# Optimization experiments

Hardware: AMD Instinct MI355X
Metric: run time of the kernel (lower is better)

The kernel has to match this reference:

```python
import jax, jax.numpy as jnp
import numpy as np

N, E, H, L = 50000, 600000, 128, 4  # nodes, edges, hidden_dim, num_layers


def setup_inputs() -> dict:
    key = jax.random.key(0)
    ks = jax.random.split(key, 12)
    def w(k, shape):
        fan_in = shape[-2]
        return jax.random.normal(k, shape, jnp.float32) / np.float32(np.sqrt(fan_in))
    return {
        "loc": jax.random.normal(ks[0], (N, 3), jnp.float32),
        "vel": jax.random.normal(ks[1], (N, 3), jnp.float32),
        "edge_attr": jax.random.normal(ks[2], (E, 2), jnp.float32),
        "row": jax.random.randint(ks[3], (E,), 0, N),
        "col": jax.random.randint(ks[4], (E,), 0, N),
        # embedding: Linear(6 -> H)
        "emb_w": w(ks[5], (6, H)), "emb_b": jnp.zeros((H,), jnp.float32),
        # per-layer edge MLP: Linear(2H+2 -> H), SiLU, Linear(H -> H), SiLU
        "ew1": w(ks[6], (L, 2 * H + 2, H)), "eb1": jnp.zeros((L, H), jnp.float32),
        "ew2": w(ks[7], (L, H, H)), "eb2": jnp.zeros((L, H), jnp.float32),
        # per-layer node MLP: Linear(2H -> H), SiLU, Linear(H -> H)
        "nw1": w(ks[8], (L, 2 * H, H)), "nb1": jnp.zeros((L, H), jnp.float32),
        "nw2": w(ks[9], (L, H, H)), "nb2": jnp.zeros((L, H), jnp.float32),
        # decoder: Linear(H -> H), SiLU, Linear(H -> 3)
        "dw1": w(ks[10], (H, H)), "db1": jnp.zeros((H,), jnp.float32),
        "dw2": w(ks[11], (H, 3)), "db2": jnp.zeros((3,), jnp.float32),
    }


def reference(loc, vel, edge_attr, row, col, emb_w, emb_b, ew1, eb1, ew2, eb2,
              nw1, nb1, nw2, nb2, dw1, db1, dw2, db2):
    silu = jax.nn.silu
    # embedding of [loc, vel]
    h = jnp.concatenate([loc, vel], axis=1) @ emb_w + emb_b  # [N, H]
    for i in range(L):
        # edge model: gather endpoints, concat edge_attr, 2-layer SiLU MLP
        e_in = jnp.concatenate([h[row], h[col], edge_attr], axis=1)  # [E, 2H+2]
        m = silu(silu(e_in @ ew1[i] + eb1[i]) @ ew2[i] + eb2[i])     # [E, H]
        # node model: scatter-sum messages into source nodes (row), MLP, residual
        agg = jax.ops.segment_sum(m, row, num_segments=N)            # [N, H]
        upd = silu(jnp.concatenate([h, agg], axis=1) @ nw1[i] + nb1[i]) @ nw2[i] + nb2[i]
        h = h + upd  # recurrent=True
    return silu(h @ dw1 + db1) @ dw2 + db2  # [N, 3]
```

## Files before the change

kernel.cpp:

```cpp
#include <hip/hip_runtime.h>

#define NN 50000
#define NE 600000
#define HD 128
#define NL 4
#define NSCB 196

typedef __bf16 bf16x8 __attribute__((ext_vector_type(8)));
typedef float f32x4 __attribute__((ext_vector_type(4)));

__device__ __forceinline__ unsigned short f2bf(float x){
  union { float f; unsigned int u; } v; v.f = x;
  unsigned int r = v.u + 0x7FFFu + ((v.u >> 16) & 1u);
  return (unsigned short)(r >> 16);
}
__device__ __forceinline__ float silu_f(float x){
  float e, r;
  float t = x * -1.44269504088896340736f;
  asm("v_exp_f32 %0, %1" : "=v"(e) : "v"(t));
  float d = 1.f + e;
  asm("v_rcp_f32 %0, %1" : "=v"(r) : "v"(d));
  return x * r;
}
__device__ __forceinline__ unsigned pk_bf16(float v0, float v1){
  unsigned r;
  asm("v_cvt_pk_bf16_f32 %0, %1, %2" : "=v"(r) : "v"(v0), "v"(v1));
  return r;
}

__device__ __forceinline__ f32x4 mfma_b16(bf16x8 a, bf16x8 b, f32x4 c){
  return __builtin_amdgcn_mfma_f32_16x16x32_bf16(a, b, c, 0, 0, 0);
}

typedef __attribute__((address_space(1))) const unsigned int* gas1p;
typedef __attribute__((address_space(3))) unsigned int* las3p;
__device__ __forceinline__ void gll16(const void* g, void* l){
  __builtin_amdgcn_global_load_lds((gas1p)g, (las3p)l, 16, 0, 0);
}

__global__ __launch_bounds__(256) void pack_b(const float* __restrict__ src,
    unsigned short* __restrict__ dst, int K, int Klimit, int srcLayerStride, int perm){
  int layer = blockIdx.y;
  int tid = blockIdx.x*256 + threadIdx.x;
  int j = tid & 7, lane = (tid >> 3) & 63, nb = (tid >> 9) & 7, kk = tid >> 12;
  int krow = (kk << 5) + ((lane >> 4) << 3) + j;
  int ll = lane & 15;
  int c = perm ? (((((nb >> 1) << 4) + ll) << 1) + (nb & 1)) : ((nb << 4) + ll);
  float v = (krow < Klimit) ? src[(size_t)layer*srcLayerStride + krow*HD + c] : 0.f;
  dst[(size_t)layer*K*HD + tid] = f2bf(v);
}

__global__ __launch_bounds__(256) void emb_kernel(
    const float* __restrict__ loc, const float* __restrict__ vel,
    const float* __restrict__ ew, const float* __restrict__ eb,
    float* __restrict__ hf, unsigned short* __restrict__ hb)
{
  int gid = blockIdx.x*256 + threadIdx.x;
  int n = gid >> 7, j = gid & 127;
  float s = eb[j];
  s += loc[n*3+0]*ew[0*HD+j] + loc[n*3+1]*ew[1*HD+j] + loc[n*3+2]*ew[2*HD+j];
  s += vel[n*3+0]*ew[3*HD+j] + vel[n*3+1]*ew[4*HD+j] + vel[n*3+2]*ew[5*HD+j];
  hf[gid] = s;
  hb[gid] = f2bf(s);
}

__global__ __launch_bounds__(256) void count_kernel(const int* __restrict__ rowIdx, int* __restrict__ cnt){
  int e = blockIdx.x*256 + threadIdx.x;
  if (e < NE) atomicAdd(cnt + rowIdx[e], 1);
}

__global__ __launch_bounds__(256) void blocksum_kernel(const int* __restrict__ cnt, int* __restrict__ bsum){
  __shared__ int s[256];
  int t = threadIdx.x, i = blockIdx.x*256 + t;
  s[t] = (i < NN) ? cnt[i] : 0;
  __syncthreads();
  for (int d = 128; d > 0; d >>= 1){
    if (t < d) s[t] += s[t + d];
    __syncthreads();
  }
  if (t == 0) bsum[blockIdx.x] = s[0];
}

__global__ __launch_bounds__(256) void scanb_kernel(int* __restrict__ bsum){
  __shared__ int s[256];
  int t = threadIdx.x;
  int v = (t < NSCB) ? bsum[t] : 0;
  s[t] = v;
  __syncthreads();
  for (int d = 1; d < 256; d <<= 1){
    int u = (t >= d) ? s[t-d] : 0;
    __syncthreads();
    s[t] += u;
    __syncthreads();
  }
  if (t < NSCB) bsum[t] = s[t] - v;
}

__global__ __launch_bounds__(256) void offsets_kernel(const int* __restrict__ cnt,
    const int* __restrict__ bsum, int* __restrict__ cur){
  __shared__ int s[256];
  int t = threadIdx.x, i = blockIdx.x*256 + t;
  int v = (i < NN) ? cnt[i] : 0;
  s[t] = v;
  __syncthreads();
  for (int d = 1; d < 256; d <<= 1){
    int u = (t >= d) ? s[t-d] : 0;
    __syncthreads();
    s[t] += u;
    __syncthreads();
  }
  if (i < NN) cur[i] = bsum[blockIdx.x] + s[t] - v;
}

__global__ __launch_bounds__(256) void assign_kernel(
    const int* __restrict__ rowIdx, const int* __restrict__ colIdx,
    const float* __restrict__ ea, int* __restrict__ cur,
    int* __restrict__ row_s, int* __restrict__ col_s, float* __restrict__ ea_s){
  int e = blockIdx.x*256 + threadIdx.x;
  if (e < NE){
    int r = rowIdx[e];
    int s = atomicAdd(cur + r, 1);
    int s64 = s & 63;
    int sp = (s & ~63) | (((s64 >> 2) & 3) << 4) | (((s64 >> 4) & 3) << 2) | (s64 & 3);
    row_s[sp] = r;
    col_s[sp] = colIdx[e];
    ea_s[2*sp]   = ea[2*e];
    ea_s[2*sp+1] = ea[2*e+1];
  }
}

#define SWZ(a) ((a) ^ (((a) >> 4) & 0x30))

__global__ __launch_bounds__(256, 8) void edge_kernel(
    const unsigned short* __restrict__ hb,
    const int* __restrict__ row_s, const int* __restrict__ col_s,
    const float* __restrict__ ea_s,
    const unsigned short* __restrict__ B1p, const unsigned short* __restrict__ B2p,
    const float* __restrict__ bias1, const float* __restrict__ bias2,
    const float* __restrict__ wea,
    float* __restrict__ aggf)
{
  __shared__ alignas(128) char sA[1024*16];
  __shared__ int sRow[64];
  __shared__ float2 sEa[64];
  uint4* sA4 = reinterpret_cast<uint4*>(sA);

  const int t = threadIdx.x;
  const int w = t >> 6, l = t & 63, lw = l >> 4, ll = l & 15;
  const int e0 = blockIdx.x << 6;

  if (t < 64){
    sRow[t] = row_s[e0 + t];
    sEa[t] = reinterpret_cast<const float2*>(ea_s)[e0 + t];
  }
  const int er = e0 + (w << 4) + ll;
  const int nrow = row_s[er];
  const int ncol = col_s[er];
  const unsigned short* gr = hb + (size_t)nrow*HD + (lw << 3);
  #pragma unroll
  for (int kk = 0; kk < 4; ++kk)
    gll16(gr + (kk << 5), sA + ((size_t)(((kk << 2) + w)) << 10));
  asm volatile("s_waitcnt vmcnt(0)" ::: "memory");
  __syncthreads();

  const int q2 = ((w << 4) + ll) << 1;
  const float2 bb1 = *reinterpret_cast<const float2*>(bias1 + q2);
  const float2 wA = *reinterpret_cast<const float2*>(wea + q2);
  const float2 wB = *reinterpret_cast<const float2*>(wea + HD + q2);

  f32x4 acc[4][2] = {};
  #pragma unroll
  for (int kk = 0; kk < 4; ++kk){
    bf16x8 a[4], b[2];
    #pragma unroll
    for (int r = 0; r < 4; ++r)
      a[r] = *reinterpret_cast<const bf16x8*>(&sA4[((kk << 2) + r)*64 + l]);
    #pragma unroll
    for (int c = 0; c < 2; ++c)
      b[c] = *reinterpret_cast<const bf16x8*>(B1p + ((((kk << 3) + (w << 1) + c) << 6) + l)*8);
    #pragma unroll
    for (int r = 0; r < 4; ++r)
      #pragma unroll
      for (int c = 0; c < 2; ++c)
        acc[r][c] = mfma_b16(a[r], b[c], acc[r][c]);
  }
  __syncthreads();

  const unsigned short* gc = hb + (size_t)ncol*HD + (lw << 3);
  #pragma unroll
  for (int kk = 0; kk < 4; ++kk)
    gll16(gc + (kk << 5), sA + ((size_t)(((kk << 2) + w)) << 10));
  asm volatile("s_waitcnt vmcnt(0)" ::: "memory");
  __syncthreads();

  #pragma unroll
  for (int kk = 4; kk < 8; ++kk){
    bf16x8 a[4], b[2];
    #pragma unroll
    for (int r = 0; r < 4; ++r)
      a[r] = *reinterpret_cast<const bf16x8*>(&sA4[(((kk - 4) << 2) + r)*64 + l]);
    #pragma unroll
    for (int c = 0; c < 2; ++c)
      b[c] = *reinterpret_cast<const bf16x8*>(B1p + ((((kk << 3) + (w << 1) + c) << 6) + l)*8);
    #pragma unroll
    for (int r = 0; r < 4; ++r)
      #pragma unroll
      for (int c = 0; c < 2; ++c)
        acc[r][c] = mfma_b16(a[r], b[c], acc[r][c]);
  }
  __syncthreads();

  #pragma unroll
  for (int r = 0; r < 4; ++r){
    #pragma unroll
    for (int i = 0; i < 4; ++i){
      int rt = (r << 4) + (lw << 2) + i;
      float2 eav = sEa[rt];
      float v0 = silu_f(acc[r][0][i] + bb1.x + eav.x*wA.x + eav.y*wB.x);
      float v1 = silu_f(acc[r][1][i] + bb1.y + eav.x*wA.y + eav.y*wB.y);
      unsigned d = pk_bf16(v0, v1);
      int a0 = ((((w << 2) + r) << 10) | ((ll >> 2) << 8) | (lw << 6) | (i << 4) | ((ll & 3) << 2));
      *reinterpret_cast<unsigned*>(sA + SWZ(a0)) = d;
    }
  }
  __syncthreads();

  f32x4 acc2[4][2] = {};
  #pragma unroll
  for (int kk = 0; kk < 4; ++kk){
    bf16x8 a[4], b[2];
    #pragma unroll
    for (int r = 0; r < 4; ++r){
      int a0 = ((((kk << 2) + r) << 10) | (l << 4));
      a[r] = *reinterpret_cast<const bf16x8*>(sA + SWZ(a0));
    }
    #pragma unroll
    for (int c = 0; c < 2; ++c)
      b[c] = *reinterpret_cast<const bf16x8*>(B2p + ((((kk << 3) + (w << 1) + c) << 6) + l)*8);
    #pragma unroll
    for (int r = 0; r < 4; ++r)
      #pragma unroll
      for (int c = 0; c < 2; ++c)
        acc2[r][c] = mfma_b16(a[r], b[c], acc2[r][c]);
  }

  {
    const int col0 = (w << 5) + ll;
    const float b20 = bias2[col0], b21 = bias2[col0 + 16];
    int curNode = -1;
    float s0 = 0.f, s1 = 0.f;
    #pragma unroll
    for (int r = 0; r < 4; ++r){
      #pragma unroll
      for (int i = 0; i < 4; ++i){
        int rt = (r << 4) + (lw << 2) + i;
        int nd = sRow[rt];
        float v0 = silu_f(acc2[r][0][i] + b20);
        float v1 = silu_f(acc2[r][1][i] + b21);
        if (nd != curNode){
          if (curNode >= 0){
            atomicAdd(aggf + (size_t)curNode*HD + col0,      s0);
            atomicAdd(aggf + (size_t)curNode*HD + col0 + 16, s1);
          }
          curNode = nd; s0 = v0; s1 = v1;
        } else { s0 += v0; s1 += v1; }
      }
    }
    atomicAdd(aggf + (size_t)curNode*HD + col0,      s0);
    atomicAdd(aggf + (size_t)curNode*HD + col0 + 16, s1);
  }
}

__global__ __launch_bounds__(256, 8) void node_kernel(
    unsigned short* hb, float* aggf,
    const unsigned short* __restrict__ B1p, const unsigned short* __restrict__ B2p,
    const float* __restrict__ bias1, const float* __restrict__ bias2,
    float* hf)
{
  __shared__ alignas(128) char sA[1024*16];
  uint4* sA4 = reinterpret_cast<uint4*>(sA);
  const int t = threadIdx.x;
  const int w = t >> 6, l = t & 63, lw = l >> 4, ll = l & 15;
  const int n0 = blockIdx.x << 6;

  const int nlane = n0 + (w << 4) + ll;
  const int ncl = (nlane < NN) ? nlane : 0;
  const unsigned short* gh = hb + (size_t)ncl*HD + (lw << 3);
  #pragma unroll
  for (int kk = 0; kk < 4; ++kk)
    gll16(gh + (kk << 5), sA + ((size_t)(((kk << 2) + w)) << 10));
  asm volatile("s_waitcnt vmcnt(0)" ::: "memory");
  __syncthreads();

  const int q2 = ((w << 4) + ll) << 1;
  const float2 bb1 = *reinterpret_cast<const float2*>(bias1 + q2);

  f32x4 acc[4][2] = {};
  #pragma unroll
  for (int kk = 0; kk < 4; ++kk){
    bf16x8 a[4], b[2];
    #pragma unroll
    for (int r = 0; r < 4; ++r)
      a[r] = *reinterpret_cast<const bf16x8*>(&sA4[((kk << 2) + r)*64 + l]);
    #pragma unroll
    for (int c = 0; c < 2; ++c)
      b[c] = *reinterpret_cast<const bf16x8*>(B1p + ((((kk << 3) + (w << 1) + c) << 6) + l)*8);
    #pragma unroll
    for (int r = 0; r < 4; ++r)
      #pragma unroll
      for (int c = 0; c < 2; ++c)
        acc[r][c] = mfma_b16(a[r], b[c], acc[r][c]);
  }
  __syncthreads();

  {
    float* gaf = aggf + (size_t)ncl*HD + (lw << 3);
    #pragma unroll
    for (int kk = 0; kk < 4; ++kk){
      float4 f0 = *reinterpret_cast<const float4*>(gaf + (kk << 5));
      float4 f1 = *reinterpret_cast<const float4*>(gaf + (kk << 5) + 4);
      uint4 d;
      d.x = pk_bf16(f0.x, f0.y);
      d.y = pk_bf16(f0.z, f0.w);
      d.z = pk_bf16(f1.x, f1.y);
      d.w = pk_bf16(f1.z, f1.w);
      *reinterpret_cast<uint4*>(sA + ((size_t)(((kk << 2) + w)) << 10) + (l << 4)) = d;
    }
    if (nlane < NN){
      const float4 z4 = make_float4(0.f, 0.f, 0.f, 0.f);
      #pragma unroll
      for (int kk = 0; kk < 4; ++kk){
        *reinterpret_cast<float4*>(gaf + (kk << 5)) = z4;
        *reinterpret_cast<float4*>(gaf + (kk << 5) + 4) = z4;
      }
    }
  }
  __syncthreads();

  #pragma unroll
  for (int kk = 4; kk < 8; ++kk){
    bf16x8 a[4], b[2];
    #pragma unroll
    for (int r = 0; r < 4; ++r)
      a[r] = *reinterpret_cast<const bf16x8*>(&sA4[(((kk - 4) << 2) + r)*64 + l]);
    #pragma unroll
    for (int c = 0; c < 2; ++c)
      b[c] = *reinterpret_cast<const bf16x8*>(B1p + ((((kk << 3) + (w << 1) + c) << 6) + l)*8);
    #pragma unroll
    for (int r = 0; r < 4; ++r)
      #pragma unroll
      for (int c = 0; c < 2; ++c)
        acc[r][c] = mfma_b16(a[r], b[c], acc[r][c]);
  }
  __syncthreads();

  #pragma unroll
  for (int r = 0; r < 4; ++r){
    #pragma unroll
    for (int i = 0; i < 4; ++i){
      unsigned d = pk_bf16(silu_f(acc[r][0][i] + bb1.x), silu_f(acc[r][1][i] + bb1.y));
      int a0 = ((((w << 2) + r) << 10) | ((ll >> 2) << 8) | (lw << 6) | (i << 4) | ((ll & 3) << 2));
      *reinterpret_cast<unsigned*>(sA + SWZ(a0)) = d;
    }
  }
  __syncthreads();

  f32x4 acc2[4][2] = {};
  #pragma unroll
  for (int kk = 0; kk < 4; ++kk){
    bf16x8 a[4], b[2];
    #pragma unroll
    for (int r = 0; r < 4; ++r){
      int a0 = ((((kk << 2) + r) << 10) | (l << 4));
      a[r] = *reinterpret_cast<const bf16x8*>(sA + SWZ(a0));
    }
    #pragma unroll
    for (int c = 0; c < 2; ++c)
      b[c] = *reinterpret_cast<const bf16x8*>(B2p + ((((kk << 3) + (w << 1) + c) << 6) + l)*8);
    #pragma unroll
    for (int r = 0; r < 4; ++r)
      #pragma unroll
      for (int c = 0; c < 2; ++c)
        acc2[r][c] = mfma_b16(a[r], b[c], acc2[r][c]);
  }

  {
    const float2 bb2 = *reinterpret_cast<const float2*>(bias2 + q2);
    #pragma unroll
    for (int r = 0; r < 4; ++r){
      #pragma unroll
      for (int i = 0; i < 4; ++i){
        int rt = (r << 4) + (lw << 2) + i;
        int n = n0 + rt;
        if (n < NN){
          float2 ho = *reinterpret_cast<const float2*>(hf + (size_t)n*HD + q2);
          float h0 = ho.x + acc2[r][0][i] + bb2.x;
          float h1 = ho.y + acc2[r][1][i] + bb2.y;
          *reinterpret_cast<float2*>(hf + (size_t)n*HD + q2) = make_float2(h0, h1);
          *reinterpret_cast<unsigned*>(hb + (size_t)n*HD + q2) = pk_bf16(h0, h1);
        }
      }
    }
  }
}

__global__ __launch_bounds__(256) void dec_kernel(
    const unsigned short* __restrict__ hb, const unsigned short* __restrict__ D1p,
    const float* __restrict__ db1, const float* __restrict__ dw2,
    const float* __restrict__ db2, float* __restrict__ outp)
{
  __shared__ alignas(128) char sA[1024*16];
  uint4* sA4 = reinterpret_cast<uint4*>(sA);
  __shared__ float sT[64*133];
  const int t = threadIdx.x;
  const int n0 = blockIdx.x << 6;
  {
    const int nl_ = t >> 2, p = t & 3;
    const int n = n0 + nl_;
    const bool valid = (n < NN);
    const int nc = valid ? n : 0;
    const uint4* src = reinterpret_cast<const uint4*>(hb + (size_t)nc*HD);
    const int base16 = ((nl_ >> 4) << 6) + (nl_ & 15);
    #pragma unroll
    for (int c = 0; c < 4; ++c){
      int q = (p << 2) + c;
      uint4 d = valid ? src[q] : make_uint4(0,0,0,0);
      sA4[base16 + ((q >> 2) << 8) + ((q & 3) << 4)] = d;
    }
  }
  __syncthreads();

  const int w = t >> 6, l = t & 63;
  const int lw = l >> 4, ll = l & 15;

  f32x4 acc[4][2] = {};
  #pragma unroll
  for (int kk = 0; kk < 4; ++kk){
    bf16x8 a[4], b[2];
    #pragma unroll
    for (int r = 0; r < 4; ++r)
      a[r] = *reinterpret_cast<const bf16x8*>(&sA4[((kk << 2) + r)*64 + l]);
    #pragma unroll
    for (int c = 0; c < 2; ++c)
      b[c] = *reinterpret_cast<const bf16x8*>(D1p + ((((kk << 3) + (w << 1) + c) << 6) + l)*8);
    #pragma unroll
    for (int r = 0; r < 4; ++r)
      #pragma unroll
      for (int c = 0; c < 2; ++c)
        acc[r][c] = mfma_b16(a[r], b[c], acc[r][c]);
  }
  #pragma unroll
  for (int r = 0; r < 4; ++r){
    #pragma unroll
    for (int i = 0; i < 4; ++i){
      int rt = (r << 4) + (lw << 2) + i;
      #pragma unroll
      for (int c = 0; c < 2; ++c){
        int col = (w << 5) + (c << 4) + ll;
        sT[rt*133 + col] = silu_f(acc[r][c][i] + db1[col]);
      }
    }
  }
  __syncthreads();
  if (t < 192){
    int rr = t & 63, cc = t >> 6;
    int n = n0 + rr;
    if (n < NN){
      float s = db2[cc];
      #pragma unroll 8
      for (int k = 0; k < HD; ++k) s += sT[rr*133 + k]*dw2[k*3 + cc];
      outp[(size_t)n*3 + cc] = s;
    }
  }
}

static inline char* alignup(char* p, size_t a){ return (char*)(((uintptr_t)p + a - 1) & ~(a - 1)); }

extern "C" void kernel_launch(void* const* d_in, const int* in_sizes, int n_in,
                              void* d_out, int out_size, void* d_ws, size_t ws_size,
                              hipStream_t stream)
{
  const float* loc  = (const float*)d_in[0];
  const float* vel  = (const float*)d_in[1];
  const float* ea   = (const float*)d_in[2];
  const int*   row  = (const int*)d_in[3];
  const int*   col  = (const int*)d_in[4];
  const float* embw = (const float*)d_in[5];
  const float* embb = (const float*)d_in[6];
  const float* ew1  = (const float*)d_in[7];
  const float* eb1  = (const float*)d_in[8];
  const float* ew2  = (const float*)d_in[9];
  const float* eb2  = (const float*)d_in[10];
  const float* nw1  = (const float*)d_in[11];
  const float* nb1  = (const float*)d_in[12];
  const float* nw2  = (const float*)d_in[13];
  const float* nb2  = (const float*)d_in[14];
  const float* dw1  = (const float*)d_in[15];
  const float* db1  = (const float*)d_in[16];
  const float* dw2  = (const float*)d_in[17];
  const float* db2  = (const float*)d_in[18];

  char* p = (char*)d_ws;
  float* hf = (float*)p;                       p += (size_t)NN*HD*4;
  unsigned short* hbuf = (unsigned short*)p;   p += (size_t)NN*HD*2;
  float* aggf = (float*)p;                     p += (size_t)NN*HD*4;
  int* cnt = (int*)p;                          p += (size_t)NN*4;
  int* cur = (int*)p;                          p += (size_t)NN*4;
  int* bsum = (int*)p;                         p += (size_t)256*4;   p = alignup(p, 256);
  int* row_s = (int*)p;                        p += (size_t)NE*4;
  int* col_s = (int*)p;                        p += (size_t)NE*4;
  float* ea_s = (float*)p;                     p += (size_t)NE*2*4;
  unsigned short* ew1p = (unsigned short*)p;   p += (size_t)NL*256*HD*2;
  unsigned short* ew2p = (unsigned short*)p;   p += (size_t)NL*128*HD*2;
  unsigned short* nw1p = (unsigned short*)p;   p += (size_t)NL*256*HD*2;
  unsigned short* nw2p = (unsigned short*)p;   p += (size_t)NL*128*HD*2;
  unsigned short* dw1p = (unsigned short*)p;   p += (size_t)128*HD*2;

  hipMemsetAsync(cnt, 0, (size_t)NN*4, stream);
  count_kernel<<<(NE + 255)/256, 256, 0, stream>>>(row, cnt);
  blocksum_kernel<<<NSCB, 256, 0, stream>>>(cnt, bsum);
  scanb_kernel<<<1, 256, 0, stream>>>(bsum);
  offsets_kernel<<<NSCB, 256, 0, stream>>>(cnt, bsum, cur);
  assign_kernel<<<(NE + 255)/256, 256, 0, stream>>>(row, col, ea, cur, row_s, col_s, ea_s);

  pack_b<<<dim3(128, NL), 256, 0, stream>>>(ew1, ew1p, 256, 256, 258*HD, 1);
  pack_b<<<dim3(64,  NL), 256, 0, stream>>>(ew2, ew2p, 128, 128, 128*HD, 0);
  pack_b<<<dim3(128, NL), 256, 0, stream>>>(nw1, nw1p, 256, 256, 256*HD, 1);
  pack_b<<<dim3(64,  NL), 256, 0, stream>>>(nw2, nw2p, 128, 128, 128*HD, 1);
  pack_b<<<dim3(64,  1 ), 256, 0, stream>>>(dw1, dw1p, 128, 128, 0, 0);

  emb_kernel<<<(NN*HD)/256, 256, 0, stream>>>(loc, vel, embw, embb, hf, hbuf);

  hipMemsetAsync(aggf, 0, (size_t)NN*HD*4, stream);
  for (int i = 0; i < NL; ++i){
    edge_kernel<<<NE/64, 256, 0, stream>>>(hbuf, row_s, col_s, ea_s,
        ew1p + (size_t)i*256*HD, ew2p + (size_t)i*128*HD,
        eb1 + i*HD, eb2 + i*HD,
        ew1 + (size_t)i*258*HD + 256*HD, aggf);
    node_kernel<<<(NN + 63)/64, 256, 0, stream>>>(hbuf, aggf,
        nw1p + (size_t)i*256*HD, nw2p + (size_t)i*128*HD,
        nb1 + i*HD, nb2 + i*HD, hf);
  }

  dec_kernel<<<(NN + 63)/64, 256, 0, stream>>>(hbuf, dw1p, db1, dw2, db2, (float*)d_out);
}
```

Before: 618.3 us.

## Pack edge records into int4 and simplify scatter flush, reuse accumulators

Replaces the separate row, col and edge-attribute arrays with one 16-byte record per edge, so the edge kernel fetches row and col with a single int2 load and the attributes with one vector load. The segmented scatter now checks whether the next edge's destination node differs, instead of tracking the current node, which removes the trailing flush. Both MLP kernels reuse the first accumulator array for the second GEMM to reduce register pressure. The gain is likely small, since the edge index loads are a minor share of the traffic next to the gathers of hidden rows.

```diff
diff --git a/kernel.cpp b/kernel.cpp
--- a/kernel.cpp
+++ b/kernel.cpp
@@ -115,17 +115,15 @@
 __global__ __launch_bounds__(256) void assign_kernel(
     const int* __restrict__ rowIdx, const int* __restrict__ colIdx,
     const float* __restrict__ ea, int* __restrict__ cur,
-    int* __restrict__ row_s, int* __restrict__ col_s, float* __restrict__ ea_s){
+    int4* __restrict__ erec){
   int e = blockIdx.x*256 + threadIdx.x;
   if (e < NE){
     int r = rowIdx[e];
     int s = atomicAdd(cur + r, 1);
     int s64 = s & 63;
     int sp = (s & ~63) | (((s64 >> 2) & 3) << 4) | (((s64 >> 4) & 3) << 2) | (s64 & 3);
-    row_s[sp] = r;
-    col_s[sp] = colIdx[e];
-    ea_s[2*sp]   = ea[2*e];
-    ea_s[2*sp+1] = ea[2*e+1];
+    float2 eav = reinterpret_cast<const float2*>(ea)[e];
+    erec[sp] = make_int4(r, colIdx[e], __float_as_int(eav.x), __float_as_int(eav.y));
   }
 }
 
@@ -133,8 +131,7 @@
 
 __global__ __launch_bounds__(256, 8) void edge_kernel(
     const unsigned short* __restrict__ hb,
-    const int* __restrict__ row_s, const int* __restrict__ col_s,
-    const float* __restrict__ ea_s,
+    const int4* __restrict__ erec,
     const unsigned short* __restrict__ B1p, const unsigned short* __restrict__ B2p,
     const float* __restrict__ bias1, const float* __restrict__ bias2,
     const float* __restrict__ wea,
@@ -150,13 +147,13 @@
   const int e0 = blockIdx.x << 6;
 
   if (t < 64){
-    sRow[t] = row_s[e0 + t];
-    sEa[t] = reinterpret_cast<const float2*>(ea_s)[e0 + t];
+    int4 rec = erec[e0 + t];
+    sRow[t] = rec.x;
+    sEa[t] = make_float2(__int_as_float(rec.z), __int_as_float(rec.w));
   }
   const int er = e0 + (w << 4) + ll;
-  const int nrow = row_s[er];
-  const int ncol = col_s[er];
-  const unsigned short* gr = hb + (size_t)nrow*HD + (lw << 3);
+  const int2 rc = *reinterpret_cast<const int2*>(&erec[er]);
+  const unsigned short* gr = hb + (size_t)rc.x*HD + (lw << 3);
   #pragma unroll
   for (int kk = 0; kk < 4; ++kk)
     gll16(gr + (kk << 5), sA + ((size_t)(((kk << 2) + w)) << 10));
@@ -186,7 +183,7 @@
   }
   __syncthreads();
 
-  const unsigned short* gc = hb + (size_t)ncol*HD + (lw << 3);
+  const unsigned short* gc = hb + (size_t)rc.y*HD + (lw << 3);
   #pragma unroll
   for (int kk = 0; kk < 4; ++kk)
     gll16(gc + (kk << 5), sA + ((size_t)(((kk << 2) + w)) << 10));
@@ -225,7 +222,12 @@
   }
   __syncthreads();
 
-  f32x4 acc2[4][2] = {};
+  #pragma unroll
+  for (int r = 0; r < 4; ++r)
+    #pragma unroll
+    for (int c = 0; c < 2; ++c)
+      acc[r][c] = (f32x4){0.f, 0.f, 0.f, 0.f};
+
   #pragma unroll
   for (int kk = 0; kk < 4; ++kk){
     bf16x8 a[4], b[2];
@@ -241,13 +243,12 @@
     for (int r = 0; r < 4; ++r)
       #pragma unroll
       for (int c = 0; c < 2; ++c)
-        acc2[r][c] = mfma_b16(a[r], b[c], acc2[r][c]);
+        acc[r][c] = mfma_b16(a[r], b[c], acc[r][c]);
   }
 
   {
     const int col0 = (w << 5) + ll;
     const float b20 = bias2[col0], b21 = bias2[col0 + 16];
-    int curNode = -1;
     float s0 = 0.f, s1 = 0.f;
     #pragma unroll
     for (int r = 0; r < 4; ++r){
@@ -255,19 +256,17 @@
       for (int i = 0; i < 4; ++i){
         int rt = (r << 4) + (lw << 2) + i;
         int nd = sRow[rt];
-        float v0 = silu_f(acc2[r][0][i] + b20);
-        float v1 = silu_f(acc2[r][1][i] + b21);
-        if (nd != curNode){
-          if (curNode >= 0){
-            atomicAdd(aggf + (size_t)curNode*HD + col0,      s0);
-            atomicAdd(aggf + (size_t)curNode*HD + col0 + 16, s1);
-          }
-          curNode = nd; s0 = v0; s1 = v1;
-        } else { s0 += v0; s1 += v1; }
+        s0 += silu_f(acc[r][0][i] + b20);
+        s1 += silu_f(acc[r][1][i] + b21);
+        bool flush = (r == 3 && i == 3) ||
+                     (sRow[(i == 3) ? (rt + 13) : (rt + 1)] != nd);
+        if (flush){
+          atomicAdd(aggf + (size_t)nd*HD + col0,      s0);
+          atomicAdd(aggf + (size_t)nd*HD + col0 + 16, s1);
+          s0 = 0.f; s1 = 0.f;
+        }
       }
     }
-    atomicAdd(aggf + (size_t)curNode*HD + col0,      s0);
-    atomicAdd(aggf + (size_t)curNode*HD + col0 + 16, s1);
   }
 }
 
@@ -365,7 +364,12 @@
   }
   __syncthreads();
 
-  f32x4 acc2[4][2] = {};
+  #pragma unroll
+  for (int r = 0; r < 4; ++r)
+    #pragma unroll
+    for (int c = 0; c < 2; ++c)
+      acc[r][c] = (f32x4){0.f, 0.f, 0.f, 0.f};
+
   #pragma unroll
   for (int kk = 0; kk < 4; ++kk){
     bf16x8 a[4], b[2];
@@ -381,7 +385,7 @@
     for (int r = 0; r < 4; ++r)
       #pragma unroll
       for (int c = 0; c < 2; ++c)
-        acc2[r][c] = mfma_b16(a[r], b[c], acc2[r][c]);
+        acc[r][c] = mfma_b16(a[r], b[c], acc[r][c]);
   }
 
   {
@@ -394,8 +398,8 @@
         int n = n0 + rt;
         if (n < NN){
           float2 ho = *reinterpret_cast<const float2*>(hf + (size_t)n*HD + q2);
-          float h0 = ho.x + acc2[r][0][i] + bb2.x;
-          float h1 = ho.y + acc2[r][1][i] + bb2.y;
+          float h0 = ho.x + acc[r][0][i] + bb2.x;
+          float h1 = ho.y + acc[r][1][i] + bb2.y;
           *reinterpret_cast<float2*>(hf + (size_t)n*HD + q2) = make_float2(h0, h1);
           *reinterpret_cast<unsigned*>(hb + (size_t)n*HD + q2) = pk_bf16(h0, h1);
         }
@@ -507,9 +511,7 @@
   int* cnt = (int*)p;                          p += (size_t)NN*4;
   int* cur = (int*)p;                          p += (size_t)NN*4;
   int* bsum = (int*)p;                         p += (size_t)256*4;   p = alignup(p, 256);
-  int* row_s = (int*)p;                        p += (size_t)NE*4;
-  int* col_s = (int*)p;                        p += (size_t)NE*4;
-  float* ea_s = (float*)p;                     p += (size_t)NE*2*4;
+  int4* erec = (int4*)p;                       p += (size_t)NE*16;
   unsigned short* ew1p = (unsigned short*)p;   p += (size_t)NL*256*HD*2;
   unsigned short* ew2p = (unsigned short*)p;   p += (size_t)NL*128*HD*2;
   unsigned short* nw1p = (unsigned short*)p;   p += (size_t)NL*256*HD*2;
@@ -521,7 +523,7 @@
   blocksum_kernel<<<NSCB, 256, 0, stream>>>(cnt, bsum);
   scanb_kernel<<<1, 256, 0, stream>>>(bsum);
   offsets_kernel<<<NSCB, 256, 0, stream>>>(cnt, bsum, cur);
-  assign_kernel<<<(NE + 255)/256, 256, 0, stream>>>(row, col, ea, cur, row_s, col_s, ea_s);
+  assign_kernel<<<(NE + 255)/256, 256, 0, stream>>>(row, col, ea, cur, erec);
 
   pack_b<<<dim3(128, NL), 256, 0, stream>>>(ew1, ew1p, 256, 256, 258*HD, 1);
   pack_b<<<dim3(64,  NL), 256, 0, stream>>>(ew2, ew2p, 128, 128, 128*HD, 0);
@@ -533,7 +535,7 @@
 
   hipMemsetAsync(aggf, 0, (size_t)NN*HD*4, stream);
   for (int i = 0; i < NL; ++i){
-    edge_kernel<<<NE/64, 256, 0, stream>>>(hbuf, row_s, col_s, ea_s,
+    edge_kernel<<<NE/64, 256, 0, stream>>>(hbuf, erec,
         ew1p + (size_t)i*256*HD, ew2p + (size_t)i*128*HD,
         eb1 + i*HD, eb2 + i*HD,
         ew1 + (size_t)i*258*HD + 256*HD, aggf);
```

Result: no change. 627.3 us (+1.5%).

## Accumulate edge messages in bf16 with packed atomics and remap blocks per XCD

Applied to the files above, without the earlier changes.

Edge messages are now scatter-added into a bf16 aggregation buffer with packed global_atomic_pk_add_bf16, where before they went into an fp32 buffer through scalar atomics. The ew2 pack permutation is changed so each lane holds adjacent output columns, which the packed atomic requires. The node kernel loads the bf16 aggregate straight into LDS with global_load_lds and zeroes it, instead of converting from fp32. Edge blocks are also remapped so contiguous (row-sorted) edge ranges land on the same XCD, which should improve L2 locality for the atomics. The cost is lower accumulation precision: summing bf16 across many edges may lose accuracy.

```diff
diff --git a/kernel.cpp b/kernel.cpp
--- a/kernel.cpp
+++ b/kernel.cpp
@@ -5,6 +5,7 @@
 #define HD 128
 #define NL 4
 #define NSCB 196
+#define NWG_E (NE/64)
 
 typedef __bf16 bf16x8 __attribute__((ext_vector_type(8)));
 typedef float f32x4 __attribute__((ext_vector_type(4)));
@@ -26,6 +27,10 @@
   unsigned r;
   asm("v_cvt_pk_bf16_f32 %0, %1, %2" : "=v"(r) : "v"(v0), "v"(v1));
   return r;
+}
+__device__ __forceinline__ void atomic_pk_add_bf16(unsigned short* addr, unsigned data){
+  asm volatile("global_atomic_pk_add_bf16 %0, %1, off"
+    :: "v"((unsigned long long)(uintptr_t)addr), "v"(data) : "memory");
 }
 
 __device__ __forceinline__ f32x4 mfma_b16(bf16x8 a, bf16x8 b, f32x4 c){
@@ -138,7 +143,7 @@
     const unsigned short* __restrict__ B1p, const unsigned short* __restrict__ B2p,
     const float* __restrict__ bias1, const float* __restrict__ bias2,
     const float* __restrict__ wea,
-    float* __restrict__ aggf)
+    unsigned short* __restrict__ aggb)
 {
   __shared__ alignas(128) char sA[1024*16];
   __shared__ int sRow[64];
@@ -147,7 +152,12 @@
 
   const int t = threadIdx.x;
   const int w = t >> 6, l = t & 63, lw = l >> 4, ll = l & 15;
-  const int e0 = blockIdx.x << 6;
+
+  int orig = blockIdx.x;
+  int xcd = orig & 7, idx = orig >> 3;
+  const int qq = NWG_E >> 3, rr = NWG_E & 7;
+  int bid = (xcd < rr) ? xcd*(qq + 1) + idx : rr*(qq + 1) + (xcd - rr)*qq + idx;
+  const int e0 = bid << 6;
 
   if (t < 64){
     sRow[t] = row_s[e0 + t];
@@ -245,8 +255,7 @@
   }
 
   {
-    const int col0 = (w << 5) + ll;
-    const float b20 = bias2[col0], b21 = bias2[col0 + 16];
+    const float2 bb2 = *reinterpret_cast<const float2*>(bias2 + q2);
     int curNode = -1;
     float s0 = 0.f, s1 = 0.f;
     #pragma unroll
@@ -255,24 +264,21 @@
       for (int i = 0; i < 4; ++i){
         int rt = (r << 4) + (lw << 2) + i;
         int nd = sRow[rt];
-        float v0 = silu_f(acc2[r][0][i] + b20);
-        float v1 = silu_f(acc2[r][1][i] + b21);
+        float v0 = silu_f(acc2[r][0][i] + bb2.x);
+        float v1 = silu_f(acc2[r][1][i] + bb2.y);
         if (nd != curNode){
-          if (curNode >= 0){
-            atomicAdd(aggf + (size_t)curNode*HD + col0,      s0);
-            atomicAdd(aggf + (size_t)curNode*HD + col0 + 16, s1);
-          }
+          if (curNode >= 0)
+            atomic_pk_add_bf16(aggb + (size_t)curNode*HD + q2, pk_bf16(s0, s1));
           curNode = nd; s0 = v0; s1 = v1;
         } else { s0 += v0; s1 += v1; }
       }
     }
-    atomicAdd(aggf + (size_t)curNode*HD + col0,      s0);
-    atomicAdd(aggf + (size_t)curNode*HD + col0 + 16, s1);
+    atomic_pk_add_bf16(aggb + (size_t)curNode*HD + q2, pk_bf16(s0, s1));
   }
 }
 
 __global__ __launch_bounds__(256, 8) void node_kernel(
-    unsigned short* hb, float* aggf,
+    unsigned short* hb, unsigned short* aggb,
     const unsigned short* __restrict__ B1p, const unsigned short* __restrict__ B2p,
     const float* __restrict__ bias1, const float* __restrict__ bias2,
     float* hf)
@@ -313,27 +319,16 @@
   }
   __syncthreads();
 
-  {
-    float* gaf = aggf + (size_t)ncl*HD + (lw << 3);
-    #pragma unroll
-    for (int kk = 0; kk < 4; ++kk){
-      float4 f0 = *reinterpret_cast<const float4*>(gaf + (kk << 5));
-      float4 f1 = *reinterpret_cast<const float4*>(gaf + (kk << 5) + 4);
-      uint4 d;
-      d.x = pk_bf16(f0.x, f0.y);
-      d.y = pk_bf16(f0.z, f0.w);
-      d.z = pk_bf16(f1.x, f1.y);
-      d.w = pk_bf16(f1.z, f1.w);
-      *reinterpret_cast<uint4*>(sA + ((size_t)(((kk << 2) + w)) << 10) + (l << 4)) = d;
-    }
-    if (nlane < NN){
-      const float4 z4 = make_float4(0.f, 0.f, 0.f, 0.f);
-      #pragma unroll
-      for (int kk = 0; kk < 4; ++kk){
-        *reinterpret_cast<float4*>(gaf + (kk << 5)) = z4;
-        *reinterpret_cast<float4*>(gaf + (kk << 5) + 4) = z4;
-      }
-    }
+  unsigned short* ga = aggb + (size_t)ncl*HD + (lw << 3);
+  #pragma unroll
+  for (int kk = 0; kk < 4; ++kk)
+    gll16(ga + (kk << 5), sA + ((size_t)(((kk << 2) + w)) << 10));
+  asm volatile("s_waitcnt vmcnt(0)" ::: "memory");
+  if (nlane < NN){
+    const uint4 z4 = make_uint4(0u, 0u, 0u, 0u);
+    #pragma unroll
+    for (int kk = 0; kk < 4; ++kk)
+      *reinterpret_cast<uint4*>(ga + (kk << 5)) = z4;
   }
   __syncthreads();
 
@@ -503,7 +498,7 @@
   char* p = (char*)d_ws;
   float* hf = (float*)p;                       p += (size_t)NN*HD*4;
   unsigned short* hbuf = (unsigned short*)p;   p += (size_t)NN*HD*2;
-  float* aggf = (float*)p;                     p += (size_t)NN*HD*4;
+  unsigned short* aggb = (unsigned short*)p;   p += (size_t)NN*HD*2;
   int* cnt = (int*)p;                          p += (size_t)NN*4;
   int* cur = (int*)p;                          p += (size_t)NN*4;
   int* bsum = (int*)p;                         p += (size_t)256*4;   p = alignup(p, 256);
@@ -524,20 +519,20 @@
   assign_kernel<<<(NE + 255)/256, 256, 0, stream>>>(row, col, ea, cur, row_s, col_s, ea_s);
 
   pack_b<<<dim3(128, NL), 256, 0, stream>>>(ew1, ew1p, 256, 256, 258*HD, 1);
-  pack_b<<<dim3(64,  NL), 256, 0, stream>>>(ew2, ew2p, 128, 128, 128*HD, 0);
+  pack_b<<<dim3(64,  NL), 256, 0, stream>>>(ew2, ew2p, 128, 128, 128*HD, 1);
   pack_b<<<dim3(128, NL), 256, 0, stream>>>(nw1, nw1p, 256, 256, 256*HD, 1);
   pack_b<<<dim3(64,  NL), 256, 0, stream>>>(nw2, nw2p, 128, 128, 128*HD, 1);
   pack_b<<<dim3(64,  1 ), 256, 0, stream>>>(dw1, dw1p, 128, 128, 0, 0);
 
   emb_kernel<<<(NN*HD)/256, 256, 0, stream>>>(loc, vel, embw, embb, hf, hbuf);
 
-  hipMemsetAsync(aggf, 0, (size_t)NN*HD*4, stream);
+  hipMemsetAsync(aggb, 0, (size_t)NN*HD*2, stream);
   for (int i = 0; i < NL; ++i){
-    edge_kernel<<<NE/64, 256, 0, stream>>>(hbuf, row_s, col_s, ea_s,
+    edge_kernel<<<NWG_E, 256, 0, stream>>>(hbuf, row_s, col_s, ea_s,
         ew1p + (size_t)i*256*HD, ew2p + (size_t)i*128*HD,
         eb1 + i*HD, eb2 + i*HD,
-        ew1 + (size_t)i*258*HD + 256*HD, aggf);
-    node_kernel<<<(NN + 63)/64, 256, 0, stream>>>(hbuf, aggf,
+        ew1 + (size_t)i*258*HD + 256*HD, aggb);
+    node_kernel<<<(NN + 63)/64, 256, 0, stream>>>(hbuf, aggb,
         nw1p + (size_t)i*256*HD, nw2p + (size_t)i*128*HD,
         nb1 + i*HD, nb2 + i*HD, hf);
   }
```

Result: faster. 586.5 us, median of 3 (-5.1%).
